# Kernel tuning notes

Hardware: AMD Instinct MI355X
Metric: run time of the kernel (lower is better)

The kernel has to match this reference:

```python
import jax, jax.numpy as jnp
import numpy as np
from jax import lax


def _hard_sigmoid(x):
    # keras hard_sigmoid: clip(0.2*x + 0.5, 0, 1)
    return jnp.clip(0.2 * x + 0.5, 0.0, 1.0)


def setup_inputs() -> dict:
    key = jax.random.key(0)
    ks = jax.random.split(key, 7)
    B, T, D, U = 64, 512, 512, 512
    s = 0.05  # keep activations in a sane range
    return {
        "x": jax.random.normal(ks[0], (B, T, D), dtype=jnp.float32),
        "h0": jnp.zeros((B, U), dtype=jnp.float32),
        "wr": jax.random.normal(ks[1], (D + U, U), dtype=jnp.float32) * s,
        "wz": jax.random.normal(ks[2], (D + U, U), dtype=jnp.float32) * s,
        "wh": jax.random.normal(ks[3], (D + U, U), dtype=jnp.float32) * s,
        "br": jax.random.normal(ks[4], (U,), dtype=jnp.float32) * s,
        "bz": jax.random.normal(ks[5], (U,), dtype=jnp.float32) * s,
        "bh": jax.random.normal(ks[6], (U,), dtype=jnp.float32) * s,
    }


def reference(x, h0, wr, wz, wh, br, bz, bh):
    """GRU over the time dim; returns final hidden state [B, U].

    Per-step math matches My_GRU_Cell.call: state h is concatenated FIRST
    ([h, x_t]), gates use hard_sigmoid, candidate uses tanh,
    h_t = h*(1-z) + z*h_hat.
    """

    def step(h, xt):
        hx = jnp.concatenate([h, xt], axis=-1)          # [B, U+D]
        rt = _hard_sigmoid(hx @ wr + br)                # [B, U]
        zt = _hard_sigmoid(hx @ wz + bz)                # [B, U]
        rhx = jnp.concatenate([h * rt, xt], axis=-1)    # [B, U+D]
        ht_hat = jnp.tanh(rhx @ wh + bh)                # [B, U]
        ht = h * (1.0 - zt) + zt * ht_hat
        return ht, None

    xs = jnp.swapaxes(x, 0, 1)  # [T, B, D]
    hT, _ = lax.scan(step, h0, xs)
    return hT
```

## Files before the change

### kernel.cpp

```cpp
#include <hip/hip_runtime.h>
#include <hip/hip_fp16.h>

typedef _Float16 f16;
typedef _Float16 half8 __attribute__((ext_vector_type(8)));
typedef float f32x4 __attribute__((ext_vector_type(4)));
typedef unsigned int u32;
typedef unsigned long long u64;
typedef unsigned short u16;

#define WCOLS 96
#define WROWB 1040
#define LDS_W (WCOLS * WROWB)
#define LDS_A (16 * WROWB)
#define LDS_H (16 * 33 * 4)
#define LDS_REC (LDS_W + LDS_A + LDS_H + 32)

#define A_ADD32(p, v)  __hip_atomic_fetch_add((u32*)(p), (u32)(v), __ATOMIC_RELAXED, __HIP_MEMORY_SCOPE_AGENT)
#define SYS_LD32(p)    __hip_atomic_load((const u32*)(p), __ATOMIC_RELAXED, __HIP_MEMORY_SCOPE_SYSTEM)
#define SYS_LD64(p)    __hip_atomic_load((const u64*)(p), __ATOMIC_RELAXED, __HIP_MEMORY_SCOPE_SYSTEM)
#define SYS_ST32(p, v) __hip_atomic_store((u32*)(p), (u32)(v), __ATOMIC_RELAXED, __HIP_MEMORY_SCOPE_SYSTEM)
#define SYS_ST64(p, v) __hip_atomic_store((u64*)(p), (u64)(v), __ATOMIC_RELAXED, __HIP_MEMORY_SCOPE_SYSTEM)

static __device__ __forceinline__ void tcc_swap32(u32* p, u32 v) {
  asm volatile("global_atomic_swap %0, %1, off" :: "v"(p), "v"(v) : "memory");
}
static __device__ __forceinline__ void tcc_swap64(u64* p, u64 v) {
  asm volatile("global_atomic_swap_x2 %0, %1, off" :: "v"(p), "v"(v) : "memory");
}
static __device__ __forceinline__ u32 tcc_add_ret0(u32* p) {
  u32 ret;
  asm volatile("global_atomic_add %0, %1, %2, off sc0\n\ts_waitcnt vmcnt(0)"
               : "=&v"(ret) : "v"(p), "v"(0u) : "memory");
  return ret;
}
static __device__ __forceinline__ u32 sc1_ld32(const u32* p) {
  u32 r;
  asm volatile("global_load_dword %0, %1, off sc1\n\ts_waitcnt vmcnt(0)"
               : "=v"(r) : "v"(p) : "memory");
  return r;
}
static __device__ __forceinline__ void sysld_u16_issue(u32& dst, const void* p) {
  asm volatile("global_load_ushort %0, %1, off sc0 sc1"
               : "=v"(dst) : "v"(p) : "memory");
}


__global__ void probe_xcd_k(u32* syncb) {
  if (threadIdx.x == 0) {
    u32 xcc;
    asm volatile("s_getreg_b32 %0, hwreg(HW_REG_XCC_ID)" : "=s"(xcc));
    __hip_atomic_fetch_add(syncb + (xcc & 7u), 1u, __ATOMIC_RELAXED,
                           __HIP_MEMORY_SCOPE_AGENT);
  }
}

__global__ void cvt_weights_k(const float* __restrict__ wr, const float* __restrict__ wz,
                              const float* __restrict__ wh, f16* __restrict__ WT) {
  int k = blockIdx.x;
  int gate = blockIdx.y;
  int c = threadIdx.x;
  const float* w = (gate == 0) ? wr : (gate == 1) ? wz : wh;
  WT[((size_t)(gate * 512 + c)) * 1024 + k] = (f16)w[(size_t)k * 512 + c];
}

__global__ __launch_bounds__(256) void precompute_x_k(
    const float* __restrict__ x, const f16* __restrict__ WT,
    const float* __restrict__ br, const float* __restrict__ bz,
    const float* __restrict__ bh, f16* __restrict__ pre) {
  __shared__ char As[64 * 80];
  __shared__ char Bs[256 * 80];
  const int m0 = blockIdx.x * 64;
  const int n0 = blockIdx.y * 256;
  const int tid = threadIdx.x;
  const int lane = tid & 63;
  const int w = tid >> 6;
  f32x4 acc[16];
#pragma unroll
  for (int i = 0; i < 16; ++i) acc[i] = (f32x4){0.f, 0.f, 0.f, 0.f};

  for (int kk = 0; kk < 16; ++kk) {
    {
      int row = tid >> 2, kc = (tid & 3) * 8;
      const float* s = x + (size_t)(m0 + row) * 512 + kk * 32 + kc;
      float4 v0 = ((const float4*)s)[0];
      float4 v1 = ((const float4*)s)[1];
      half8 h;
      h[0] = (f16)v0.x; h[1] = (f16)v0.y; h[2] = (f16)v0.z; h[3] = (f16)v0.w;
      h[4] = (f16)v1.x; h[5] = (f16)v1.y; h[6] = (f16)v1.z; h[7] = (f16)v1.w;
      *(half8*)(As + row * 80 + kc * 2) = h;
      const uint4* bsrc = (const uint4*)(WT + ((size_t)(n0 + tid)) * 1024 + 512 + kk * 32);
      uint4* bdst = (uint4*)(Bs + tid * 80);
      bdst[0] = bsrc[0]; bdst[1] = bsrc[1]; bdst[2] = bsrc[2]; bdst[3] = bsrc[3];
    }
    __syncthreads();
    half8 a = *(const half8*)(As + (w * 16 + (lane & 15)) * 80 + (lane >> 4) * 16);
#pragma unroll
    for (int nt = 0; nt < 16; ++nt) {
      half8 b = *(const half8*)(Bs + (nt * 16 + (lane & 15)) * 80 + (lane >> 4) * 16);
      acc[nt] = __builtin_amdgcn_mfma_f32_16x16x32_f16(a, b, acc[nt], 0, 0, 0);
    }
    __syncthreads();
  }
#pragma unroll
  for (int nt = 0; nt < 16; ++nt) {
    int col = n0 + nt * 16 + (lane & 15);
    int gate = col >> 9, ci = col & 511;
    float bias = ((gate == 0) ? br : (gate == 1) ? bz : bh)[ci];
#pragma unroll
    for (int r = 0; r < 4; ++r) {
      int m = m0 + w * 16 + (lane >> 4) * 4 + r;
      int b = m >> 9, t = m & 511;
      pre[((size_t)t * 64 + b) * 1536 + col] = (f16)(acc[nt][r] + bias);
    }
  }
}

__global__ __launch_bounds__(256, 1) void gru_rec_k(
    const f16* __restrict__ WT, const f16* __restrict__ pre,
    const float* __restrict__ h0, f16* h16, f16* hr16,
    u32* syncb, float* __restrict__ out) {
  extern __shared__ char smem[];
  char* Wl = smem;
  char* Al = smem + LDS_W;
  float* Hl = (float*)(smem + LDS_W + LDS_A);
  volatile int* s_misc = (int*)(smem + LDS_W + LDS_A + LDS_H);
  const int tid = threadIdx.x;
  const int lane = tid & 63;
  const int w = tid >> 6;

  if (tid == 0) {
    u32 xcc;
    asm volatile("s_getreg_b32 %0, hwreg(HW_REG_XCC_ID)" : "=s"(xcc));
    xcc &= 7u;
    int trusted = 1;
    for (int i = 0; i < 8; ++i)
      if (SYS_LD32(syncb + i) < 16u) trusted = 0;
    int g = 0, cb = 0, mode = 0;
    if (trusted) {
      u32 slot = A_ADD32(syncb + 8 + xcc, 1u);
      if (xcc < 4u && slot < 16u) { g = (int)xcc; cb = (int)slot; mode = 2; }
    } else {
      u32 slot = A_ADD32(syncb + 16, 1u);
      if (slot < 64u) { g = (int)(slot & 3u); cb = (int)(slot >> 2); mode = 1; }
    }
    s_misc[0] = g; s_misc[1] = cb; s_misc[2] = mode;
    s_misc[3] = 0; s_misc[4] = 1; s_misc[5] = 0;
  }
  __syncthreads();
  const int mode = s_misc[2];
  if (mode == 0) return;
  const int g = s_misc[0];
  const int cb = s_misc[1];

  u32* cnt     = syncb + 64 + g * 32;
  u32* tcnt    = syncb + 256 + g * 32;
  u32* verds   = syncb + 512 + g * 512;
  u32* l2slots = syncb + 4096 + g * 512;
  u32* tsts    = syncb + 6144 + g * 512;
  u32* abortf  = syncb + 24;

  auto gbar = [&](u32* c, u32 target) -> int {
    __syncthreads();
    if (tid == 0) {
      A_ADD32(c, 1u);
      u32 it = 0;
      while (SYS_LD32(c) < 16u * target) {
        __builtin_amdgcn_s_sleep(1);
        if (((++it) & 63u) == 0u) {
          if (SYS_LD32(abortf) != 0u) { s_misc[3] = 1; break; }
          if (it > 400000u) { A_ADD32(abortf, 1u); s_misc[3] = 1; break; }
        }
      }
    }
    __syncthreads();
    return s_misc[3];
  };

  int l2m = 0, ab = 0;
  if (mode == 2) {
    u32* mytst = tsts + cb * 32;
    if (tid == 0) tcc_swap32(mytst, 0xA5000000u | (u32)cb);
    ab = gbar(tcnt, 1u);
    if (!ab) {
      if (tid < 16) {
        u32 v = sc1_ld32(tsts + tid * 32);
        if (v != (0xA5000000u | (u32)tid)) s_misc[4] = 0;
      }
      __syncthreads();
      if (tid == 0) tcc_swap32(mytst, 0x5A000000u | (u32)cb);
      ab = gbar(tcnt, 2u);
    }
    if (!ab) {
      if (tid < 16) {
        u32 v = sc1_ld32(tsts + tid * 32);
        if (v != (0x5A000000u | (u32)tid)) s_misc[4] = 0;
        u32 v2 = tcc_add_ret0(tsts + tid * 32);
        if (v2 != (0x5A000000u | (u32)tid)) s_misc[4] = 0;
      }
      __syncthreads();
      if (tid == 0) SYS_ST32(verds + cb * 32, 1u + (u32)s_misc[4]);
      ab = gbar(tcnt, 3u);
      if (tid == 0) s_misc[5] = 1;
      __syncthreads();
      if (tid < 16) {
        if (SYS_LD32(verds + tid * 32) != 2u) s_misc[5] = 0;
      }
      __syncthreads();
      l2m = s_misc[5];
    }
  }

  auto barK = [&](u32 target, bool keep) -> int {
    if (!l2m) return gbar(cnt, target);
    if (keep) asm volatile("s_waitcnt vmcnt(8) lgkmcnt(0)" ::: "memory");
    else      asm volatile("s_waitcnt vmcnt(0) lgkmcnt(0)" ::: "memory");
    __builtin_amdgcn_sched_barrier(0);
    __builtin_amdgcn_s_barrier();
    if (tid == 0) tcc_swap32(l2slots + cb * 32, target);
    if (tid < 64) {
      u32* pl = l2slots + (lane & 15) * 32;
      u32 it = 0;
      for (;;) {
        bool ok = true;
        if (lane < 16) ok = (tcc_add_ret0(pl) >= target);
        if (__all(ok)) break;
        if (((++it) & 63u) == 0u) {
          if (SYS_LD32(abortf) != 0u) { if (lane == 0) s_misc[3] = 1; break; }
          if (it > 200000u) { SYS_ST32(abortf, 1u); if (lane == 0) s_misc[3] = 1; break; }
        }
      }
    }
    asm volatile("s_waitcnt lgkmcnt(0)" ::: "memory");
    __builtin_amdgcn_s_barrier();
    __builtin_amdgcn_sched_barrier(0);
    return s_misc[3];
  };

  for (int i = tid; i < WCOLS * 64; i += 256) {
    int lc = i >> 6, c16 = i & 63;
    int gate = lc / 32, ci = cb * 32 + (lc & 31);
    const uint4* s = (const uint4*)(WT + ((size_t)(gate * 512 + ci)) * 1024) + c16;
    *(uint4*)(Wl + lc * WROWB + c16 * 16) = *s;
  }
  for (int i = tid; i < 16 * 32; i += 256) {
    int row = i >> 5, c = i & 31;
    Hl[row * 33 + c] = h0[(size_t)(g * 16 + row) * 512 + cb * 32 + c];
  }
  if (cb == 0) {
    u64* dst = (u64*)(h16 + (size_t)g * 16 * 512);
    for (int i = tid; i < 2048; i += 256) {
      int e0 = i * 4;
      const float* hp = h0 + (size_t)(g * 16 + (e0 >> 9)) * 512 + (e0 & 511);
      u16 b0 = __builtin_bit_cast(u16, (f16)hp[0]);
      u16 b1 = __builtin_bit_cast(u16, (f16)hp[1]);
      u16 b2 = __builtin_bit_cast(u16, (f16)hp[2]);
      u16 b3 = __builtin_bit_cast(u16, (f16)hp[3]);
      u64 v = (u64)b0 | ((u64)b1 << 16) | ((u64)b2 << 32) | ((u64)b3 << 48);
      if (l2m) tcc_swap64(dst + i, v); else SYS_ST64(dst + i, v);
    }
  }

  const int rq = lane >> 4;
  const int lc1 = w * 16 + (lane & 15);
  const int ci1 = cb * 32 + (lc1 & 31);
  const int gcol1 = (lc1 < 32) ? ci1 : (512 + ci1);
  const int lch = (w >= 2) ? ((w - 2) * 16 + (lane & 15)) : 0;
  const int ci2 = cb * 32 + lch;
  const char* Ab  = Al + (lane & 15) * WROWB + rq * 16;
  const char* Bb1 = Wl + lc1 * WROWB + rq * 16;
  const char* Bb2 = Wl + (64 + lch) * WROWB + rq * 16;
  const int gcol2 = (w >= 2) ? (1024 + ci2) : gcol1;

  u32 q1[4], q2[4];
  float p1r[4], p2r[4];
  auto issue_pre = [&](int t) {
#pragma unroll
    for (int r = 0; r < 4; ++r) {
      const int grow = g * 16 + rq * 4 + r;
      const u16* base = (const u16*)pre + ((size_t)t * 64 + grow) * 1536;
      sysld_u16_issue(q1[r], base + gcol1);
      sysld_u16_issue(q2[r], base + gcol2);
    }
  };
  auto convert_pre = [&]() {
#pragma unroll
    for (int r = 0; r < 4; ++r) {
      p1r[r] = (float)__builtin_bit_cast(f16, (u16)(q1[r] & 0xffffu));
      p2r[r] = (float)__builtin_bit_cast(f16, (u16)(q2[r] & 0xffffu));
    }
  };

  auto stage = [&](const f16* src16) {
    if (l2m) {
      const char* s = (const char*)src16;
      uint4 t0, t1, t2, t3;
      asm volatile(
          "global_load_dwordx4 %0, %4, off sc1\n\t"
          "global_load_dwordx4 %1, %5, off sc1\n\t"
          "global_load_dwordx4 %2, %6, off sc1\n\t"
          "global_load_dwordx4 %3, %7, off sc1\n\t"
          "s_waitcnt vmcnt(0)"
          : "=&v"(t0), "=&v"(t1), "=&v"(t2), "=&v"(t3)
          : "v"(s + (size_t)tid * 16), "v"(s + (size_t)(256 + tid) * 16),
            "v"(s + (size_t)(512 + tid) * 16), "v"(s + (size_t)(768 + tid) * 16)
          : "memory");
      { int u = tid;       *(uint4*)(Al + (u >> 6) * WROWB + (u & 63) * 16) = t0; }
      { int u = 256 + tid; *(uint4*)(Al + (u >> 6) * WROWB + (u & 63) * 16) = t1; }
      { int u = 512 + tid; *(uint4*)(Al + (u >> 6) * WROWB + (u & 63) * 16) = t2; }
      { int u = 768 + tid; *(uint4*)(Al + (u >> 6) * WROWB + (u & 63) * 16) = t3; }
    } else {
      const u64* s = (const u64*)src16;
      u64 tmp[8];
#pragma unroll
      for (int i = 0; i < 8; ++i) tmp[i] = SYS_LD64(s + i * 256 + tid);
#pragma unroll
      for (int i = 0; i < 8; ++i) {
        int u = i * 256 + tid;
        *(u64*)(Al + (u >> 7) * WROWB + (u & 127) * 8) = tmp[i];
      }
    }
    __syncthreads();
    __builtin_amdgcn_sched_barrier(0);
  };

  auto gwrite = [&](f16* base, int grow, int ci, u32 hb_u32) {
    u32 p01 = hb_u32 | (((u32)(u16)__shfl_xor((int)hb_u32, 1, 64)) << 16);
    u64 q = (u64)p01 | (((u64)(u32)__shfl_xor((int)p01, 2, 64)) << 32);
    if (!(lane & 3)) {
      u64* dst = (u64*)(base + (size_t)grow * 512 + ci);
      if (l2m) tcc_swap64(dst, q); else SYS_ST64(dst, q);
    }
  };

  issue_pre(0);
  ab = ab ? ab : barK(1u, false);

  f32x4 zreg = {0.f, 0.f, 0.f, 0.f};
  for (int t = 0; t < 512 && !ab; ++t) {
    stage(h16 + (size_t)g * 16 * 512);
    convert_pre();
    f32x4 acc = {0.f, 0.f, 0.f, 0.f};
#pragma unroll
    for (int kk = 0; kk < 16; ++kk) {
      half8 a = *(const half8*)(Ab + kk * 64);
      half8 b = *(const half8*)(Bb1 + kk * 64);
      acc = __builtin_amdgcn_mfma_f32_16x16x32_f16(a, b, acc, 0, 0, 0);
    }
    if (lc1 < 32) {
#pragma unroll
      for (int r = 0; r < 4; ++r) {
        float v = acc[r] + p1r[r];
        float gt = fmaxf(0.f, fminf(1.f, 0.2f * v + 0.5f));
        float hv = Hl[(rq * 4 + r) * 33 + (lc1 & 31)];
        u32 hb = (u32)__builtin_bit_cast(u16, (f16)(hv * gt));
        gwrite(hr16, g * 16 + rq * 4 + r, ci1, hb);
      }
    } else {
#pragma unroll
      for (int r = 0; r < 4; ++r) {
        float v = acc[r] + p1r[r];
        zreg[r] = fmaxf(0.f, fminf(1.f, 0.2f * v + 0.5f));
      }
    }
    if (t < 511) issue_pre(t + 1);
    ab = barK(2u * t + 2u, t < 511);
    if (ab) break;
    stage(hr16 + (size_t)g * 16 * 512);
    if (w >= 2) {
      f32x4 acc2 = {0.f, 0.f, 0.f, 0.f};
#pragma unroll
      for (int kk = 0; kk < 16; ++kk) {
        half8 a = *(const half8*)(Ab + kk * 64);
        half8 b = *(const half8*)(Bb2 + kk * 64);
        acc2 = __builtin_amdgcn_mfma_f32_16x16x32_f16(a, b, acc2, 0, 0, 0);
      }
#pragma unroll
      for (int r = 0; r < 4; ++r) {
        float v = acc2[r] + p2r[r];
        float vc = fminf(9.f, fmaxf(-9.f, v));
        float e = __expf(2.f * vc);
        float hh = (e - 1.f) * __builtin_amdgcn_rcpf(e + 1.f);
        const int row = rq * 4 + r;
        float ho = Hl[row * 33 + lch];
        float z = zreg[r];
        float hn = ho * (1.f - z) + z * hh;
        Hl[row * 33 + lch] = hn;
        u32 hb = (u32)__builtin_bit_cast(u16, (f16)hn);
        gwrite(h16, g * 16 + row, ci2, hb);
        if (t == 511) out[(size_t)(g * 16 + row) * 512 + ci2] = hn;
      }
    }
    if (t < 511) ab = barK(2u * t + 3u, false);
  }
}

extern "C" void kernel_launch(void* const* d_in, const int* in_sizes, int n_in,
                              void* d_out, int out_size, void* d_ws, size_t ws_size,
                              hipStream_t stream) {
  const float* x  = (const float*)d_in[0];
  const float* h0 = (const float*)d_in[1];
  const float* wr = (const float*)d_in[2];
  const float* wz = (const float*)d_in[3];
  const float* wh = (const float*)d_in[4];
  const float* br = (const float*)d_in[5];
  const float* bz = (const float*)d_in[6];
  const float* bh = (const float*)d_in[7];
  float* out = (float*)d_out;

  char* ws = (char*)d_ws;
  size_t off = 0;
  f16* WT = (f16*)(ws + off);   off += (size_t)1536 * 1024 * 2;
  f16* pre = (f16*)(ws + off);  off += (size_t)512 * 64 * 1536 * 2;
  f16* h16 = (f16*)(ws + off);  off += (size_t)64 * 512 * 2;
  f16* hr16 = (f16*)(ws + off); off += (size_t)64 * 512 * 2;
  u32* syncb = (u32*)(ws + off); off += 32768;

  if (ws_size < off) {
    hipMemsetAsync(d_out, 0, (size_t)out_size * 4, stream);
    return;
  }

  hipMemsetAsync(syncb, 0, 32768, stream);
  probe_xcd_k<<<512, 64, 0, stream>>>(syncb);
  cvt_weights_k<<<dim3(1024, 3), 512, 0, stream>>>(wr, wz, wh, WT);
  precompute_x_k<<<dim3(512, 6), 256, 0, stream>>>(x, WT, br, bz, bh, pre);
  hipFuncSetAttribute(reinterpret_cast<const void*>(gru_rec_k),
                      hipFuncAttributeMaxDynamicSharedMemorySize, LDS_REC);
  gru_rec_k<<<1024, 256, LDS_REC, stream>>>(WT, pre, h0, h16, hr16, syncb, out);
}
```

Before: 2.705 ms.

## Replace block-wide grid barriers with per-wave producer/consumer flags and double-buffered LDS

The per-step grid barrier used a block-wide s_barrier plus a single per-block slot. It is replaced by per-wave flags: only the waves that produce a given buffer publish a flag, and each wave waits only on the producer waves it needs. The staged hidden-state buffer is split into two LDS buffers (one for h, one for r*h) so the two phases no longer overwrite each other's staging area. This is meant to cut barrier latency on the serial 512-step critical path. In exchange it uses more LDS, more sync slots and more polling traffic, and ordering becomes harder to reason about.

```diff
diff --git a/kernel.cpp b/kernel.cpp
--- a/kernel.cpp
+++ b/kernel.cpp
@@ -13,7 +13,7 @@
 #define LDS_W (WCOLS * WROWB)
 #define LDS_A (16 * WROWB)
 #define LDS_H (16 * 33 * 4)
-#define LDS_REC (LDS_W + LDS_A + LDS_H + 32)
+#define LDS_REC (LDS_W + 2 * LDS_A + LDS_H + 32)
 
 #define A_ADD32(p, v)  __hip_atomic_fetch_add((u32*)(p), (u32)(v), __ATOMIC_RELAXED, __HIP_MEMORY_SCOPE_AGENT)
 #define SYS_LD32(p)    __hip_atomic_load((const u32*)(p), __ATOMIC_RELAXED, __HIP_MEMORY_SCOPE_SYSTEM)
@@ -120,10 +120,11 @@
     const float* __restrict__ h0, f16* h16, f16* hr16,
     u32* syncb, float* __restrict__ out) {
   extern __shared__ char smem[];
-  char* Wl = smem;
-  char* Al = smem + LDS_W;
-  float* Hl = (float*)(smem + LDS_W + LDS_A);
-  volatile int* s_misc = (int*)(smem + LDS_W + LDS_A + LDS_H);
+  char* Wl  = smem;
+  char* AlA = smem + LDS_W;
+  char* AlB = smem + LDS_W + LDS_A;
+  float* Hl = (float*)(smem + LDS_W + 2 * LDS_A);
+  volatile int* s_misc = (int*)(smem + LDS_W + 2 * LDS_A + LDS_H);
   const int tid = threadIdx.x;
   const int lane = tid & 63;
   const int w = tid >> 6;
@@ -152,11 +153,12 @@
   const int g = s_misc[0];
   const int cb = s_misc[1];
 
-  u32* cnt     = syncb + 64 + g * 32;
+  u32* cnt0    = syncb + 64 + g * 32;
+  u32* cntM    = syncb + 128 + g * 32;
   u32* tcnt    = syncb + 256 + g * 32;
   u32* verds   = syncb + 512 + g * 512;
-  u32* l2slots = syncb + 4096 + g * 512;
-  u32* tsts    = syncb + 6144 + g * 512;
+  u32* l2slots = syncb + 4096 + g * 2048;
+  u32* tsts    = syncb + 12288 + g * 512;
   u32* abortf  = syncb + 24;
 
   auto gbar = [&](u32* c, u32 target) -> int {
@@ -210,30 +212,35 @@
     }
   }
 
-  auto barK = [&](u32 target, bool keep) -> int {
-    if (!l2m) return gbar(cnt, target);
-    if (keep) asm volatile("s_waitcnt vmcnt(8) lgkmcnt(0)" ::: "memory");
-    else      asm volatile("s_waitcnt vmcnt(0) lgkmcnt(0)" ::: "memory");
-    __builtin_amdgcn_sched_barrier(0);
-    __builtin_amdgcn_s_barrier();
-    if (tid == 0) tcc_swap32(l2slots + cb * 32, target);
-    if (tid < 64) {
-      u32* pl = l2slots + (lane & 15) * 32;
+  auto ap = [&](u32 target, int waitn, bool producer, u32 pmask) {
+    if (!l2m) waitn = 0;
+    if (waitn == 8)      asm volatile("s_waitcnt vmcnt(8)" ::: "memory");
+    else if (waitn == 0) asm volatile("s_waitcnt vmcnt(0)" ::: "memory");
+    if (l2m) {
+      if (lane == 0 && producer) tcc_swap32(l2slots + (cb * 4 + w) * 32, target);
+      u32* pl = l2slots + lane * 32;
+      const bool need = ((pmask >> (lane & 3)) & 1u) != 0u;
       u32 it = 0;
       for (;;) {
-        bool ok = true;
-        if (lane < 16) ok = (tcc_add_ret0(pl) >= target);
+        bool ok = !need || (sc1_ld32(pl) >= target);
         if (__all(ok)) break;
         if (((++it) & 63u) == 0u) {
-          if (SYS_LD32(abortf) != 0u) { if (lane == 0) s_misc[3] = 1; break; }
-          if (it > 200000u) { SYS_ST32(abortf, 1u); if (lane == 0) s_misc[3] = 1; break; }
+          if (SYS_LD32(abortf) != 0u) { s_misc[3] = 1; break; }
+          if (it > 100000u) { SYS_ST32(abortf, 1u); s_misc[3] = 1; break; }
         }
       }
-    }
-    asm volatile("s_waitcnt lgkmcnt(0)" ::: "memory");
-    __builtin_amdgcn_s_barrier();
-    __builtin_amdgcn_sched_barrier(0);
-    return s_misc[3];
+    } else {
+      if (lane == 0 && producer) A_ADD32(cntM, 1u);
+      u32 it = 0;
+      for (;;) {
+        bool ok = (SYS_LD32(cntM) >= 32u * (target - 1u));
+        if (__all(ok)) break;
+        if (((++it) & 63u) == 0u) {
+          if (SYS_LD32(abortf) != 0u) { s_misc[3] = 1; break; }
+          if (it > 100000u) { SYS_ST32(abortf, 1u); s_misc[3] = 1; break; }
+        }
+      }
+    }
   };
 
   for (int i = tid; i < WCOLS * 64; i += 256) {
@@ -266,7 +273,8 @@
   const int gcol1 = (lc1 < 32) ? ci1 : (512 + ci1);
   const int lch = (w >= 2) ? ((w - 2) * 16 + (lane & 15)) : 0;
   const int ci2 = cb * 32 + lch;
-  const char* Ab  = Al + (lane & 15) * WROWB + rq * 16;
+  const char* AbA = AlA + (lane & 15) * WROWB + rq * 16;
+  const char* AbB = AlB + (lane & 15) * WROWB + rq * 16;
   const char* Bb1 = Wl + lc1 * WROWB + rq * 16;
   const char* Bb2 = Wl + (64 + lch) * WROWB + rq * 16;
   const int gcol2 = (w >= 2) ? (1024 + ci2) : gcol1;
@@ -290,7 +298,7 @@
     }
   };
 
-  auto stage = [&](const f16* src16) {
+  auto stage = [&](char* Al_, const f16* src16) {
     if (l2m) {
       const char* s = (const char*)src16;
       uint4 t0, t1, t2, t3;
@@ -304,10 +312,10 @@
           : "v"(s + (size_t)tid * 16), "v"(s + (size_t)(256 + tid) * 16),
             "v"(s + (size_t)(512 + tid) * 16), "v"(s + (size_t)(768 + tid) * 16)
           : "memory");
-      { int u = tid;       *(uint4*)(Al + (u >> 6) * WROWB + (u & 63) * 16) = t0; }
-      { int u = 256 + tid; *(uint4*)(Al + (u >> 6) * WROWB + (u & 63) * 16) = t1; }
-      { int u = 512 + tid; *(uint4*)(Al + (u >> 6) * WROWB + (u & 63) * 16) = t2; }
-      { int u = 768 + tid; *(uint4*)(Al + (u >> 6) * WROWB + (u & 63) * 16) = t3; }
+      { int u = tid;       *(uint4*)(Al_ + (u >> 6) * WROWB + (u & 63) * 16) = t0; }
+      { int u = 256 + tid; *(uint4*)(Al_ + (u >> 6) * WROWB + (u & 63) * 16) = t1; }
+      { int u = 512 + tid; *(uint4*)(Al_ + (u >> 6) * WROWB + (u & 63) * 16) = t2; }
+      { int u = 768 + tid; *(uint4*)(Al_ + (u >> 6) * WROWB + (u & 63) * 16) = t3; }
     } else {
       const u64* s = (const u64*)src16;
       u64 tmp[8];
@@ -316,8 +324,9 @@
 #pragma unroll
       for (int i = 0; i < 8; ++i) {
         int u = i * 256 + tid;
-        *(u64*)(Al + (u >> 7) * WROWB + (u & 127) * 8) = tmp[i];
-      }
+        *(u64*)(Al_ + (u >> 7) * WROWB + (u & 127) * 8) = tmp[i];
+      }
+      asm volatile("s_waitcnt vmcnt(0)" ::: "memory");
     }
     __syncthreads();
     __builtin_amdgcn_sched_barrier(0);
@@ -333,16 +342,20 @@
   };
 
   issue_pre(0);
-  ab = ab ? ab : barK(1u, false);
+  if (!ab) ab = gbar(cnt0, 1u);
+
+  f16* const h16g  = h16 + (size_t)g * 16 * 512;
+  f16* const hr16g = hr16 + (size_t)g * 16 * 512;
 
   f32x4 zreg = {0.f, 0.f, 0.f, 0.f};
-  for (int t = 0; t < 512 && !ab; ++t) {
-    stage(h16 + (size_t)g * 16 * 512);
+  for (int t = 0; t < 512; ++t) {
+    stage(AlA, h16g);
+    ab = s_misc[3];
     convert_pre();
     f32x4 acc = {0.f, 0.f, 0.f, 0.f};
 #pragma unroll
     for (int kk = 0; kk < 16; ++kk) {
-      half8 a = *(const half8*)(Ab + kk * 64);
+      half8 a = *(const half8*)(AbA + kk * 64);
       half8 b = *(const half8*)(Bb1 + kk * 64);
       acc = __builtin_amdgcn_mfma_f32_16x16x32_f16(a, b, acc, 0, 0, 0);
     }
@@ -363,14 +376,15 @@
       }
     }
     if (t < 511) issue_pre(t + 1);
-    ab = barK(2u * t + 2u, t < 511);
-    if (ab) break;
-    stage(hr16 + (size_t)g * 16 * 512);
+    if (!ab)
+      ap(2u * t + 2u, (w < 2) ? ((t < 511) ? 8 : 0) : -1, w < 2, 0x3u);
+    stage(AlB, hr16g);
+    ab = s_misc[3];
     if (w >= 2) {
       f32x4 acc2 = {0.f, 0.f, 0.f, 0.f};
 #pragma unroll
       for (int kk = 0; kk < 16; ++kk) {
-        half8 a = *(const half8*)(Ab + kk * 64);
+        half8 a = *(const half8*)(AbB + kk * 64);
         half8 b = *(const half8*)(Bb2 + kk * 64);
         acc2 = __builtin_amdgcn_mfma_f32_16x16x32_f16(a, b, acc2, 0, 0, 0);
       }
@@ -390,7 +404,8 @@
         if (t == 511) out[(size_t)(g * 16 + row) * 512 + ci2] = hn;
       }
     }
-    if (t < 511) ab = barK(2u * t + 3u, false);
+    if (t < 511 && !ab)
+      ap(2u * t + 3u, (w >= 2) ? 0 : -1, w >= 2, 0xCu);
   }
 }
 
@@ -413,14 +428,14 @@
   f16* pre = (f16*)(ws + off);  off += (size_t)512 * 64 * 1536 * 2;
   f16* h16 = (f16*)(ws + off);  off += (size_t)64 * 512 * 2;
   f16* hr16 = (f16*)(ws + off); off += (size_t)64 * 512 * 2;
-  u32* syncb = (u32*)(ws + off); off += 32768;
+  u32* syncb = (u32*)(ws + off); off += 65536;
 
   if (ws_size < off) {
     hipMemsetAsync(d_out, 0, (size_t)out_size * 4, stream);
     return;
   }
 
-  hipMemsetAsync(syncb, 0, 32768, stream);
+  hipMemsetAsync(syncb, 0, 65536, stream);
   probe_xcd_k<<<512, 64, 0, stream>>>(syncb);
   cvt_weights_k<<<dim3(1024, 3), 512, 0, stream>>>(wr, wz, wh, WT);
   precompute_x_k<<<dim3(512, 6), 256, 0, stream>>>(x, WT, br, bz, bh, pre);
```

New measurement: 2.966 ms. 9.6% more time.
